# Kernel optimization log

Hardware: AMD Instinct MI355X
Metric: run time of the kernel (lower is better)

Reference implementation:

```python
import jax, jax.numpy as jnp
import numpy as np

B, T = 1, 2048
N_EMBD = 4096
N_HEAD = 32
N_GROUPS = 8
HEAD = 128
Q_PER_KV = N_HEAD // N_GROUPS  # 4
WINDOW = 1024
EPS = 1e-5
ROPE_THETA = 10000.0


def setup_inputs() -> dict:
    key = jax.random.key(0)
    k0, k1, k2 = jax.random.split(key, 3)
    x = jax.random.normal(k0, (B, T, N_EMBD), dtype=jnp.float32)
    # RoPE tables: cos/sin of shape [T, HEAD] (rotary_percentage=1.0)
    inv_freq = 1.0 / (ROPE_THETA ** (jnp.arange(0, HEAD, 2, dtype=jnp.float32) / HEAD))
    ang = jnp.arange(T, dtype=jnp.float32)[:, None] * inv_freq[None, :]  # [T, HEAD//2]
    ang = jnp.concatenate([ang, ang], axis=-1)  # [T, HEAD]
    cos, sin = jnp.cos(ang), jnp.sin(ang)
    qkv_out = (N_HEAD + 2 * N_GROUPS) * HEAD  # 6144
    W_qkv = jax.random.normal(k1, (qkv_out, N_EMBD), dtype=jnp.float32) * 0.02
    W_proj = jax.random.normal(k2, (N_EMBD, N_HEAD * HEAD), dtype=jnp.float32) * 0.02
    norm_q_w = jnp.ones((N_HEAD * HEAD,), dtype=jnp.float32)
    norm_k_w = jnp.ones((N_GROUPS * HEAD,), dtype=jnp.float32)
    return {"x": x, "cos": cos, "sin": sin, "W_qkv": W_qkv,
            "norm_q_w": norm_q_w, "norm_k_w": norm_k_w, "W_proj": W_proj}


def _rmsnorm(x, w):
    # RMSNorm over last dim, matching litgpt RMSNorm (eps inside sqrt)
    var = jnp.mean(x * x, axis=-1, keepdims=True)
    return x * jax.lax.rsqrt(var + EPS) * w


def _apply_rope(x, cos, sin):
    # x: [B, H, T, D]; cos/sin: [T, D] (broadcast over B, H)
    d = x.shape[-1]
    x1, x2 = x[..., : d // 2], x[..., d // 2:]
    rotated = jnp.concatenate([-x2, x1], axis=-1)
    return x * cos + rotated * sin


def reference(x, cos, sin, W_qkv, norm_q_w, norm_k_w, W_proj):
    Bx, Tx, _ = x.shape
    qkv = jnp.einsum('btc,oc->bto', x, W_qkv)  # [B, T, (H+2G)*D]
    q_size = N_HEAD * HEAD
    kv_size = N_GROUPS * HEAD
    q = qkv[..., :q_size]
    k = qkv[..., q_size:q_size + kv_size]
    v = qkv[..., q_size + kv_size:]
    # norm_qk: RMSNorm over the full flattened q / k dims (pre head reshape)
    q = _rmsnorm(q, norm_q_w)
    k = _rmsnorm(k, norm_k_w)
    q = q.reshape(Bx, Tx, N_HEAD, HEAD).transpose(0, 2, 1, 3)     # [B, H, T, D]
    k = k.reshape(Bx, Tx, N_GROUPS, HEAD).transpose(0, 2, 1, 3)   # [B, G, T, D]
    v = v.reshape(Bx, Tx, N_GROUPS, HEAD).transpose(0, 2, 1, 3)   # [B, G, T, D]
    # rope_n_elem == head_size (rotary_percentage = 1.0)
    q = _apply_rope(q, cos, sin)
    k = _apply_rope(k, cos, sin)
    # GQA: expand kv groups to heads (repeat_interleave on head dim)
    k = jnp.repeat(k, Q_PER_KV, axis=1)  # [B, H, T, D]
    v = jnp.repeat(v, Q_PER_KV, axis=1)
    scale = 1.0 / jnp.sqrt(jnp.float32(HEAD))  # attention_scores_scalar is None
    scores = jnp.einsum('bhqd,bhkd->bhqk', q, k) * scale
    # causal + sliding-window mask: allowed iff 0 <= q_idx - kv_idx < WINDOW
    d = jnp.arange(Tx)[:, None] - jnp.arange(Tx)[None, :]
    bias = jnp.where((d >= 0) & (d < WINDOW), 0.0, -jnp.inf).astype(scores.dtype)
    attn = jax.nn.softmax(scores + bias, axis=-1)
    y = jnp.einsum('bhqk,bhkd->bhqd', attn, v)        # [B, H, T, D]
    y = y.transpose(0, 2, 1, 3).reshape(Bx, Tx, N_HEAD * HEAD)
    return jnp.einsum('bth,oh->bto', y, W_proj)       # [B, T, n_embd]
```

## Files before the change

kernel.cpp:

```cpp
#include <hip/hip_runtime.h>
#include <stdint.h>
#include <stddef.h>

#define T_SEQ 2048
#define WINDOW_SZ 1024

typedef __attribute__((ext_vector_type(4))) float f32x4;
typedef __attribute__((ext_vector_type(16))) float f32x16;
typedef __attribute__((ext_vector_type(8))) short s16x8;
typedef __attribute__((ext_vector_type(4))) short s16x4;

__device__ inline unsigned short f2bf(float f) {
  union { float f; unsigned u; } v; v.f = f;
  unsigned u = v.u;
  return (unsigned short)((u + 0x7fffu + ((u >> 16) & 1u)) >> 16);
}
__device__ inline float bf2f(unsigned short u) {
  union { unsigned u; float f; } v; v.u = ((unsigned)u) << 16; return v.f;
}

__device__ inline void gld_lds16(const unsigned short* g, unsigned short* l) {
  __builtin_amdgcn_global_load_lds((const __attribute__((address_space(1))) void*)g,
                                   (__attribute__((address_space(3))) void*)l, 16, 0, 0);
}

__device__ inline void store_out(float* p, float v) { *p = v; }
__device__ inline void store_out(unsigned short* p, float v) { *p = f2bf(v); }

__global__ __launch_bounds__(256) void cvt_all(const float* __restrict__ x,
                                               const float* __restrict__ wqkv,
                                               const float* __restrict__ wproj,
                                               unsigned short* __restrict__ x_bf,
                                               unsigned short* __restrict__ wqkv_bf,
                                               unsigned short* __restrict__ wproj_bf) {
  int i = blockIdx.x * 256 + threadIdx.x;
  const float* s; unsigned short* d; int j;
  if (i < 2097152)       { s = x;     d = x_bf;     j = i; }
  else if (i < 8388608)  { s = wqkv;  d = wqkv_bf;  j = i - 2097152; }
  else                   { s = wproj; d = wproj_bf; j = i - 8388608; }
  float4 v = ((const float4*)s)[j];
  ushort4 o;
  o.x = f2bf(v.x); o.y = f2bf(v.y); o.z = f2bf(v.z); o.w = f2bf(v.w);
  ((ushort4*)d)[j] = o;
}

template <typename OutT>
__global__ __launch_bounds__(256) void gemm_bt(const unsigned short* __restrict__ A,
                                               const unsigned short* __restrict__ Bt,
                                               OutT* __restrict__ C, int M, int N, int K) {
  __shared__ unsigned short As[128 * 64];
  __shared__ unsigned short Bs[128 * 64];
  const int tid  = threadIdx.x;
  const int wave = tid >> 6, lane = tid & 63;
  const int l32 = lane & 31, khalf = lane >> 5;
  const int m0 = blockIdx.y << 7, n0 = blockIdx.x << 7;
  const int wr = (wave >> 1) << 6;
  const int wc = (wave & 1) << 6;
  const int srow = wave * 8 + (lane >> 3);
  const int gchunk0 = lane & 7;

  f32x16 acc[2][2] = {};

  for (int k0 = 0; k0 < K; k0 += 64) {
#pragma unroll
    for (int j = 0; j < 4; j++) {
      int r = j * 32 + srow;
      int gc = gchunk0 ^ (r & 7);
      gld_lds16(A  + (size_t)(m0 + r) * K + k0 + gc * 8, &As[(j * 32 + wave * 8) * 64]);
      gld_lds16(Bt + (size_t)(n0 + r) * K + k0 + gc * 8, &Bs[(j * 32 + wave * 8) * 64]);
    }
    __syncthreads();
#pragma unroll
    for (int s = 0; s < 4; s++) {
      s16x8 af[2], bfr[2];
      int chunk = s * 2 + khalf;
#pragma unroll
      for (int i = 0; i < 2; i++) {
        int ra = wr + i * 32 + l32;
        af[i]  = *(const s16x8*)&As[ra * 64 + ((chunk ^ (ra & 7)) * 8)];
        int rb = wc + i * 32 + l32;
        bfr[i] = *(const s16x8*)&Bs[rb * 64 + ((chunk ^ (rb & 7)) * 8)];
      }
#pragma unroll
      for (int mi = 0; mi < 2; mi++)
#pragma unroll
        for (int ni = 0; ni < 2; ni++)
          acc[mi][ni] = __builtin_amdgcn_mfma_f32_32x32x16_bf16(af[mi], bfr[ni], acc[mi][ni], 0, 0, 0);
    }
    __syncthreads();
  }
#pragma unroll
  for (int mi = 0; mi < 2; mi++)
#pragma unroll
    for (int ni = 0; ni < 2; ni++) {
      int col = n0 + wc + ni * 32 + l32;
      int rbase = m0 + wr + mi * 32 + 4 * khalf;
#pragma unroll
      for (int reg = 0; reg < 16; reg++) {
        int row = rbase + (reg & 3) + 8 * (reg >> 2);
        store_out(&C[(size_t)row * N + col], acc[mi][ni][reg]);
      }
    }
}

__device__ inline void stage_half(const unsigned short* __restrict__ g, int ldk,
                                  int grow0, int k0, unsigned short* lds,
                                  int wave, int lane) {
#pragma unroll
  for (int j = 0; j < 2; j++) {
    int rloc = j * 64 + wave * 8 + (lane >> 3);
    int lc = (lane & 7) ^ (rloc & 7);
    gld_lds16(g + (size_t)(grow0 + rloc) * ldk + k0 + lc * 8,
              lds + (j * 64 + wave * 8) * 64);
  }
}
__device__ inline void stage_64(const unsigned short* __restrict__ g, int ldk,
                                int grow0, int k0, unsigned short* lds,
                                int wave, int lane) {
  int rloc = wave * 8 + (lane >> 3);
  int lc = (lane & 7) ^ (rloc & 7);
  gld_lds16(g + (size_t)(grow0 + rloc) * ldk + k0 + lc * 8,
            lds + (wave * 8) * 64);
}

__global__ __launch_bounds__(512, 2) void gemm256(const unsigned short* __restrict__ A,
                                                  const unsigned short* __restrict__ Bt,
                                                  unsigned short* __restrict__ C,
                                                  int M, int N, int K) {
  __shared__ unsigned short S[73728];
  const int tid = threadIdx.x, wave = tid >> 6, lane = tid & 63;
  const int quad = lane >> 4, l16 = lane & 15;
  const int wm = wave >> 2, wn = wave & 3;
  const int m0 = blockIdx.y << 8, n0 = blockIdx.x * 192;
  const int NT = K >> 6;

  f32x4 acc[8][3] = {};

  unsigned short* const Ab0 = &S[0];
  unsigned short* const Bb0 = &S[49152];

  stage_half(A,  K, m0,       0, Ab0,        wave, lane);
  stage_half(A,  K, m0 + 128, 0, Ab0 + 8192, wave, lane);
  stage_half(Bt, K, n0,       0, Bb0,        wave, lane);
  stage_64  (Bt, K, n0 + 128, 0, Bb0 + 8192, wave, lane);
  if (NT > 1) {
    stage_half(A,  K, m0,       64, Ab0 + 16384,        wave, lane);
    stage_half(A,  K, m0 + 128, 64, Ab0 + 16384 + 8192, wave, lane);
    asm volatile("s_waitcnt vmcnt(4)" ::: "memory");
  } else {
    asm volatile("s_waitcnt vmcnt(0)" ::: "memory");
  }
  __builtin_amdgcn_s_barrier();
  asm volatile("" ::: "memory");

  int ac = 0;
  for (int u = 0; u < NT; ++u) {
    const unsigned short* Sa = Ab0 + ac * 16384;
    const unsigned short* Sb = Bb0 + (u & 1) * 12288;

    if (u + 1 < NT) {
      unsigned short* SbN = Bb0 + ((u + 1) & 1) * 12288;
      stage_half(Bt, K, n0,       (u + 1) << 6, SbN,        wave, lane);
      stage_64  (Bt, K, n0 + 128, (u + 1) << 6, SbN + 8192, wave, lane);
    }
    if (u + 2 < NT) {
      int an2 = ac - 1; if (an2 < 0) an2 = 2;
      unsigned short* SaN = Ab0 + an2 * 16384;
      stage_half(A, K, m0,       (u + 2) << 6, SaN,        wave, lane);
      stage_half(A, K, m0 + 128, (u + 2) << 6, SaN + 8192, wave, lane);
    }

    s16x8 bfr[3][2];
#pragma unroll
    for (int nf = 0; nf < 3; nf++)
#pragma unroll
      for (int ks = 0; ks < 2; ks++) {
        int rb = wn * 48 + nf * 16 + l16;
        bfr[nf][ks] = *(const s16x8*)&Sb[rb * 64 + (((ks * 4 + quad) ^ (rb & 7)) * 8)];
      }
    s16x8 af[8][2];
#pragma unroll
    for (int f = 0; f < 2; f++)
#pragma unroll
      for (int ks = 0; ks < 2; ks++) {
        int ra = wm * 128 + f * 16 + l16;
        af[f][ks] = *(const s16x8*)&Sa[ra * 64 + (((ks * 4 + quad) ^ (ra & 7)) * 8)];
      }
#pragma unroll
    for (int f = 0; f < 8; f++) {
      if (f < 6) {
#pragma unroll
        for (int ks = 0; ks < 2; ks++) {
          int ra = wm * 128 + (f + 2) * 16 + l16;
          af[f + 2][ks] = *(const s16x8*)&Sa[ra * 64 + (((ks * 4 + quad) ^ (ra & 7)) * 8)];
        }
      }
      __builtin_amdgcn_s_setprio(1);
#pragma unroll
      for (int nf = 0; nf < 3; nf++)
#pragma unroll
        for (int ks = 0; ks < 2; ks++)
          acc[f][nf] = __builtin_amdgcn_mfma_f32_16x16x32_bf16(
              af[f][ks], bfr[nf][ks], acc[f][nf], 0, 0, 0);
      __builtin_amdgcn_s_setprio(0);
    }

    if (u + 2 < NT) asm volatile("s_waitcnt vmcnt(4)" ::: "memory");
    else            asm volatile("s_waitcnt vmcnt(0)" ::: "memory");
    asm volatile("" ::: "memory");
    __builtin_amdgcn_s_barrier();
    asm volatile("" ::: "memory");

    ac = (ac == 2) ? 0 : ac + 1;
  }
#pragma unroll
  for (int mf = 0; mf < 8; mf++)
#pragma unroll
    for (int nf = 0; nf < 3; nf++) {
      const int row0 = m0 + wm * 128 + mf * 16 + quad * 4;
      const int col  = n0 + wn * 48 + nf * 16 + l16;
#pragma unroll
      for (int r = 0; r < 4; r++)
        C[(size_t)(row0 + r) * N + col] = f2bf(acc[mf][nf][r]);
    }
}

__global__ __launch_bounds__(256) void normrope(const unsigned short* __restrict__ qkv,
                                                const float* __restrict__ cosb,
                                                const float* __restrict__ sinb,
                                                const float* __restrict__ wq,
                                                const float* __restrict__ wk,
                                                unsigned short* __restrict__ qr,
                                                unsigned short* __restrict__ kr,
                                                unsigned short* __restrict__ vt) {
  const int t = blockIdx.x, tid = threadIdx.x;
  const unsigned short* row = qkv + (size_t)t * 6144;
  float sq = 0.f, sk = 0.f;
  {
    s16x8 a = *(const s16x8*)&row[tid * 16];
    s16x8 b = *(const s16x8*)&row[tid * 16 + 8];
#pragma unroll
    for (int j = 0; j < 8; j++) {
      float fa = bf2f((unsigned short)a[j]), fb = bf2f((unsigned short)b[j]);
      sq += fa * fa + fb * fb;
    }
  }
  {
    s16x4 a = *(const s16x4*)&row[4096 + tid * 4];
#pragma unroll
    for (int j = 0; j < 4; j++) {
      float fa = bf2f((unsigned short)a[j]);
      sk += fa * fa;
    }
  }
#pragma unroll
  for (int off = 32; off; off >>= 1) { sq += __shfl_xor(sq, off); sk += __shfl_xor(sk, off); }
  __shared__ float red[8];
  if ((tid & 63) == 0) { red[tid >> 6] = sq; red[4 + (tid >> 6)] = sk; }
  __syncthreads();
  sq = red[0] + red[1] + red[2] + red[3];
  sk = red[4] + red[5] + red[6] + red[7];
  const float rq = rsqrtf(sq * (1.f / 4096.f) + 1e-5f) * (0.08838834764831845f * 1.4426950408889634f);
  const float rk = rsqrtf(sk * (1.f / 1024.f) + 1e-5f);
  for (int i = tid; i < 4096; i += 256) {
    int h = i >> 7, d = i & 127;
    int pd = (d < 64) ? d + 64 : d - 64;
    float val = bf2f(row[i]) * rq * wq[i];
    float pv  = bf2f(row[(h << 7) + pd]) * rq * wq[(h << 7) + pd];
    float rot = (d < 64) ? -pv : pv;
    float o = val * cosb[t * 128 + d] + rot * sinb[t * 128 + d];
    qr[(size_t)h * T_SEQ * 128 + t * 128 + d] = f2bf(o);
  }
  for (int i = tid; i < 1024; i += 256) {
    int g = i >> 7, d = i & 127;
    int pd = (d < 64) ? d + 64 : d - 64;
    float val = bf2f(row[4096 + i]) * rk * wk[i];
    float pv  = bf2f(row[4096 + (g << 7) + pd]) * rk * wk[(g << 7) + pd];
    float rot = (d < 64) ? -pv : pv;
    float o = val * cosb[t * 128 + d] + rot * sinb[t * 128 + d];
    kr[(size_t)g * T_SEQ * 128 + t * 128 + d] = f2bf(o);
  }
  for (int i = tid; i < 1024; i += 256) {
    int g = i >> 7, d = i & 127;
    vt[(size_t)g * 128 * T_SEQ + (size_t)d * T_SEQ + t] = row[5120 + i];
  }
}

__global__ __launch_bounds__(512, 2) void attn(const unsigned short* __restrict__ Q,
                                               const unsigned short* __restrict__ Kb,
                                               const unsigned short* __restrict__ Vt,
                                               unsigned short* __restrict__ Y) {
  __shared__ unsigned short Kbuf[2][64 * 128];
  __shared__ unsigned short Vbuf[2][128 * 64];
  __shared__ unsigned short Pbuf[8][2][16 * 72];
  const int qb = blockIdx.x, g = blockIdx.y;
  const int tid = threadIdx.x, wave = tid >> 6, lane = tid & 63;
  const int quad = lane >> 4, l16 = lane & 15;
  const int h = g * 4 + (wave >> 1);
  const int qbase = qb * 64;
  const int q0 = qbase + (wave & 1) * 32;
  const unsigned short* Qh = Q + (size_t)h * T_SEQ * 128;
  const unsigned short* Kg = Kb + (size_t)g * T_SEQ * 128;
  const unsigned short* Vg = Vt + (size_t)g * 128 * T_SEQ;

  s16x8 aq[2][4];
#pragma unroll
  for (int qt = 0; qt < 2; qt++)
#pragma unroll
    for (int ks = 0; ks < 4; ks++)
      aq[qt][ks] = *(const s16x8*)&Qh[(size_t)(q0 + qt * 16 + l16) * 128 + ks * 32 + quad * 8];

  f32x4 acc[2][8] = {};
  float lrow[2][4] = {};

  int lo = qbase - (WINDOW_SZ - 1);
  if (lo < 0) lo = 0;
  lo &= ~63;

#define STAGE_CHUNK(buf, kkv)                                                        \
  {                                                                                  \
    int kk_ = (kkv);                                                                 \
    _Pragma("unroll")                                                                \
    for (int j = 0; j < 2; j++) {                                                    \
      int rloc = wave * 8 + j * 4 + (lane >> 4);                                     \
      int oct = (lane & 15) ^ (rloc & 15);                                           \
      gld_lds16(Kg + (size_t)(kk_ + rloc) * 128 + oct * 8,                           \
                &Kbuf[buf][(wave * 8 + j * 4) * 128]);                               \
    }                                                                                \
    _Pragma("unroll")                                                                \
    for (int j = 0; j < 2; j++) {                                                    \
      int dloc = wave * 16 + j * 8 + (lane >> 3);                                    \
      int oct = (lane & 7) ^ (dloc & 7);                                             \
      gld_lds16(Vg + (size_t)dloc * T_SEQ + kk_ + oct * 8,                           \
                &Vbuf[buf][(wave * 16 + j * 8) * 64]);                               \
    }                                                                                \
  }

  STAGE_CHUNK(0, lo);
  int ib = 0;
  for (int kk = lo; kk < qbase + 64; kk += 64, ib ^= 1) {
    __syncthreads();
    if (kk + 64 < qbase + 64) STAGE_CHUNK(ib ^ 1, kk + 64);
    if (kk > q0 + 31 || kk + 63 < q0 - (WINDOW_SZ - 1)) continue;
    const unsigned short* kb = Kbuf[ib];
    const unsigned short* vb = Vbuf[ib];
    f32x4 sc[2][4] = {};
    __builtin_amdgcn_s_setprio(1);
#pragma unroll
    for (int ks = 0; ks < 4; ks++) {
#pragma unroll
      for (int ci = 0; ci < 4; ci++) {
        s16x8 bk = *(const s16x8*)&kb[(ci * 16 + l16) * 128 + (((ks * 4 + quad) ^ l16) * 8)];
        sc[0][ci] = __builtin_amdgcn_mfma_f32_16x16x32_bf16(aq[0][ks], bk, sc[0][ci], 0, 0, 0);
        sc[1][ci] = __builtin_amdgcn_mfma_f32_16x16x32_bf16(aq[1][ks], bk, sc[1][ci], 0, 0, 0);
      }
    }
    __builtin_amdgcn_s_setprio(0);
#pragma unroll
    for (int qt = 0; qt < 2; qt++)
#pragma unroll
      for (int ci = 0; ci < 4; ci++) {
        int col = kk + ci * 16 + l16;
#pragma unroll
        for (int r = 0; r < 4; r++) {
          int irow = q0 + qt * 16 + quad * 4 + r;
          unsigned dd = (unsigned)(irow - col);
          float e = (dd < (unsigned)WINDOW_SZ) ? exp2f(sc[qt][ci][r]) : 0.f;
          lrow[qt][r] += e;
          Pbuf[wave][qt][(quad * 4 + r) * 72 + ci * 16 + l16] = f2bf(e);
        }
      }
    __builtin_amdgcn_s_setprio(1);
#pragma unroll
    for (int c = 0; c < 2; c++) {
      s16x8 pa0 = *(const s16x8*)&Pbuf[wave][0][l16 * 72 + c * 32 + quad * 8];
      s16x8 pa1 = *(const s16x8*)&Pbuf[wave][1][l16 * 72 + c * 32 + quad * 8];
#pragma unroll
      for (int n = 0; n < 8; n++) {
        s16x8 bv = *(const s16x8*)&vb[(n * 16 + l16) * 64 + (((c * 4 + quad) ^ (l16 & 7)) * 8)];
        acc[0][n] = __builtin_amdgcn_mfma_f32_16x16x32_bf16(pa0, bv, acc[0][n], 0, 0, 0);
        acc[1][n] = __builtin_amdgcn_mfma_f32_16x16x32_bf16(pa1, bv, acc[1][n], 0, 0, 0);
      }
    }
    __builtin_amdgcn_s_setprio(0);
  }
#undef STAGE_CHUNK
#pragma unroll
  for (int qt = 0; qt < 2; qt++)
#pragma unroll
    for (int r = 0; r < 4; r++) {
#pragma unroll
      for (int off = 8; off; off >>= 1) lrow[qt][r] += __shfl_xor(lrow[qt][r], off);
      lrow[qt][r] = 1.f / lrow[qt][r];
    }
#pragma unroll
  for (int qt = 0; qt < 2; qt++)
#pragma unroll
    for (int n = 0; n < 8; n++)
#pragma unroll
      for (int r = 0; r < 4; r++) {
        int irow = q0 + qt * 16 + quad * 4 + r;
        Y[(size_t)irow * 4096 + h * 128 + n * 16 + l16] = f2bf(acc[qt][n][r] * lrow[qt][r]);
      }
}

extern "C" void kernel_launch(void* const* d_in, const int* in_sizes, int n_in,
                              void* d_out, int out_size, void* d_ws, size_t ws_size,
                              hipStream_t stream) {
  (void)in_sizes; (void)n_in; (void)out_size; (void)ws_size;
  const float* x     = (const float*)d_in[0];
  const float* cosb  = (const float*)d_in[1];
  const float* sinb  = (const float*)d_in[2];
  const float* Wqkv  = (const float*)d_in[3];
  const float* wq    = (const float*)d_in[4];
  const float* wk    = (const float*)d_in[5];
  const float* Wproj = (const float*)d_in[6];
  float* out = (float*)d_out;

  char* ws = (char*)d_ws;
  unsigned short* x_bf     = (unsigned short*)(ws);
  unsigned short* wqkv_bf  = (unsigned short*)(ws + 16777216);
  unsigned short* wproj_bf = (unsigned short*)(ws + 67108864);
  unsigned short* qkv      = (unsigned short*)(ws + 100663296);
  unsigned short* qr       = (unsigned short*)(ws + 150994944);
  unsigned short* kr       = (unsigned short*)(ws + 167772160);
  unsigned short* vt       = (unsigned short*)(ws + 171966464);
  unsigned short* y        = (unsigned short*)(ws + 176160768);

  cvt_all<<<49152, 256, 0, stream>>>(x, Wqkv, Wproj, x_bf, wqkv_bf, wproj_bf);
  gemm256<<<dim3(32, 8), 512, 0, stream>>>(x_bf, wqkv_bf, qkv, 2048, 6144, 4096);
  normrope<<<2048, 256, 0, stream>>>(qkv, cosb, sinb, wq, wk, qr, kr, vt);
  attn<<<dim3(32, 8), 512, 0, stream>>>(qr, kr, vt, y);
  gemm_bt<float><<<dim3(32, 16), 256, 0, stream>>>(y, wproj_bf, out, 2048, 4096, 4096);
}
```

Before: 477.1 us.

## Replace output projection GEMM with pipelined 128x256-tile MFMA kernel

The simple 128x128 single-buffered output-projection GEMM is replaced by a 512-thread kernel with 128x256 tiles. B is triple-buffered and A double-buffered through async global-to-LDS loads, with explicit vmcnt waits and raw barriers so loads for later k-steps overlap the MFMAs of the current one. It uses 16x16x32 MFMAs with setprio around the compute and launches 256 blocks instead of 512. The goal is to hide memory latency and raise MFMA utilisation, at the cost of 128KB of LDS per block, which may limit occupancy.

```diff
diff --git a/kernel.cpp b/kernel.cpp
--- a/kernel.cpp
+++ b/kernel.cpp
@@ -23,9 +23,6 @@
   __builtin_amdgcn_global_load_lds((const __attribute__((address_space(1))) void*)g,
                                    (__attribute__((address_space(3))) void*)l, 16, 0, 0);
 }
-
-__device__ inline void store_out(float* p, float v) { *p = v; }
-__device__ inline void store_out(unsigned short* p, float v) { *p = f2bf(v); }
 
 __global__ __launch_bounds__(256) void cvt_all(const float* __restrict__ x,
                                                const float* __restrict__ wqkv,
@@ -44,65 +41,6 @@
   ((ushort4*)d)[j] = o;
 }
 
-template <typename OutT>
-__global__ __launch_bounds__(256) void gemm_bt(const unsigned short* __restrict__ A,
-                                               const unsigned short* __restrict__ Bt,
-                                               OutT* __restrict__ C, int M, int N, int K) {
-  __shared__ unsigned short As[128 * 64];
-  __shared__ unsigned short Bs[128 * 64];
-  const int tid  = threadIdx.x;
-  const int wave = tid >> 6, lane = tid & 63;
-  const int l32 = lane & 31, khalf = lane >> 5;
-  const int m0 = blockIdx.y << 7, n0 = blockIdx.x << 7;
-  const int wr = (wave >> 1) << 6;
-  const int wc = (wave & 1) << 6;
-  const int srow = wave * 8 + (lane >> 3);
-  const int gchunk0 = lane & 7;
-
-  f32x16 acc[2][2] = {};
-
-  for (int k0 = 0; k0 < K; k0 += 64) {
-#pragma unroll
-    for (int j = 0; j < 4; j++) {
-      int r = j * 32 + srow;
-      int gc = gchunk0 ^ (r & 7);
-      gld_lds16(A  + (size_t)(m0 + r) * K + k0 + gc * 8, &As[(j * 32 + wave * 8) * 64]);
-      gld_lds16(Bt + (size_t)(n0 + r) * K + k0 + gc * 8, &Bs[(j * 32 + wave * 8) * 64]);
-    }
-    __syncthreads();
-#pragma unroll
-    for (int s = 0; s < 4; s++) {
-      s16x8 af[2], bfr[2];
-      int chunk = s * 2 + khalf;
-#pragma unroll
-      for (int i = 0; i < 2; i++) {
-        int ra = wr + i * 32 + l32;
-        af[i]  = *(const s16x8*)&As[ra * 64 + ((chunk ^ (ra & 7)) * 8)];
-        int rb = wc + i * 32 + l32;
-        bfr[i] = *(const s16x8*)&Bs[rb * 64 + ((chunk ^ (rb & 7)) * 8)];
-      }
-#pragma unroll
-      for (int mi = 0; mi < 2; mi++)
-#pragma unroll
-        for (int ni = 0; ni < 2; ni++)
-          acc[mi][ni] = __builtin_amdgcn_mfma_f32_32x32x16_bf16(af[mi], bfr[ni], acc[mi][ni], 0, 0, 0);
-    }
-    __syncthreads();
-  }
-#pragma unroll
-  for (int mi = 0; mi < 2; mi++)
-#pragma unroll
-    for (int ni = 0; ni < 2; ni++) {
-      int col = n0 + wc + ni * 32 + l32;
-      int rbase = m0 + wr + mi * 32 + 4 * khalf;
-#pragma unroll
-      for (int reg = 0; reg < 16; reg++) {
-        int row = rbase + (reg & 3) + 8 * (reg >> 2);
-        store_out(&C[(size_t)row * N + col], acc[mi][ni][reg]);
-      }
-    }
-}
-
 __device__ inline void stage_half(const unsigned short* __restrict__ g, int ldk,
                                   int grow0, int k0, unsigned short* lds,
                                   int wave, int lane) {
@@ -222,6 +160,102 @@
 #pragma unroll
       for (int r = 0; r < 4; r++)
         C[(size_t)(row0 + r) * N + col] = f2bf(acc[mf][nf][r]);
+    }
+}
+
+__global__ __launch_bounds__(512, 2) void gemm256p(const unsigned short* __restrict__ A,
+                                                   const unsigned short* __restrict__ Bt,
+                                                   float* __restrict__ C,
+                                                   int M, int N, int K) {
+  __shared__ unsigned short S[65536];
+  const int tid = threadIdx.x, wave = tid >> 6, lane = tid & 63;
+  const int quad = lane >> 4, l16 = lane & 15;
+  const int wm = wave >> 2, wn = wave & 3;
+  const int m0 = blockIdx.y << 7, n0 = blockIdx.x << 8;
+  const int NT = K >> 6;
+
+  f32x4 acc[4][4] = {};
+
+  unsigned short* const Bb0 = &S[0];
+  unsigned short* const Ab0 = &S[49152];
+
+  stage_half(A,  K, m0,       0, Ab0,        wave, lane);
+  stage_half(Bt, K, n0,       0, Bb0,        wave, lane);
+  stage_half(Bt, K, n0 + 128, 0, Bb0 + 8192, wave, lane);
+  if (NT > 1) {
+    stage_half(Bt, K, n0,       64, Bb0 + 16384,        wave, lane);
+    stage_half(Bt, K, n0 + 128, 64, Bb0 + 16384 + 8192, wave, lane);
+    asm volatile("s_waitcnt vmcnt(4)" ::: "memory");
+  } else {
+    asm volatile("s_waitcnt vmcnt(0)" ::: "memory");
+  }
+  __builtin_amdgcn_s_barrier();
+  asm volatile("" ::: "memory");
+
+  int bc = 0;
+  for (int u = 0; u < NT; ++u) {
+    const unsigned short* Sb = Bb0 + bc * 16384;
+    const unsigned short* Sa = Ab0 + (u & 1) * 8192;
+
+    if (u + 1 < NT)
+      stage_half(A, K, m0, (u + 1) << 6, Ab0 + ((u + 1) & 1) * 8192, wave, lane);
+    if (u + 2 < NT) {
+      int bn2 = bc - 1; if (bn2 < 0) bn2 = 2;
+      unsigned short* SbN = Bb0 + bn2 * 16384;
+      stage_half(Bt, K, n0,       (u + 2) << 6, SbN,        wave, lane);
+      stage_half(Bt, K, n0 + 128, (u + 2) << 6, SbN + 8192, wave, lane);
+    }
+
+    s16x8 bfr[4][2];
+#pragma unroll
+    for (int nf = 0; nf < 4; nf++)
+#pragma unroll
+      for (int ks = 0; ks < 2; ks++) {
+        int rb = wn * 64 + nf * 16 + l16;
+        bfr[nf][ks] = *(const s16x8*)&Sb[rb * 64 + (((ks * 4 + quad) ^ (rb & 7)) * 8)];
+      }
+    s16x8 af[4][2];
+#pragma unroll
+    for (int ks = 0; ks < 2; ks++) {
+      int ra = wm * 64 + l16;
+      af[0][ks] = *(const s16x8*)&Sa[ra * 64 + (((ks * 4 + quad) ^ (ra & 7)) * 8)];
+    }
+#pragma unroll
+    for (int mf = 0; mf < 4; mf++) {
+      if (mf < 3) {
+#pragma unroll
+        for (int ks = 0; ks < 2; ks++) {
+          int ra = wm * 64 + (mf + 1) * 16 + l16;
+          af[mf + 1][ks] = *(const s16x8*)&Sa[ra * 64 + (((ks * 4 + quad) ^ (ra & 7)) * 8)];
+        }
+      }
+      __builtin_amdgcn_s_setprio(1);
+#pragma unroll
+      for (int nf = 0; nf < 4; nf++)
+#pragma unroll
+        for (int ks = 0; ks < 2; ks++)
+          acc[mf][nf] = __builtin_amdgcn_mfma_f32_16x16x32_bf16(
+              af[mf][ks], bfr[nf][ks], acc[mf][nf], 0, 0, 0);
+      __builtin_amdgcn_s_setprio(0);
+    }
+
+    if (u + 2 < NT) asm volatile("s_waitcnt vmcnt(4)" ::: "memory");
+    else            asm volatile("s_waitcnt vmcnt(0)" ::: "memory");
+    asm volatile("" ::: "memory");
+    __builtin_amdgcn_s_barrier();
+    asm volatile("" ::: "memory");
+
+    bc = (bc == 2) ? 0 : bc + 1;
+  }
+#pragma unroll
+  for (int mf = 0; mf < 4; mf++)
+#pragma unroll
+    for (int nf = 0; nf < 4; nf++) {
+      const int row0 = m0 + wm * 64 + mf * 16 + quad * 4;
+      const int col  = n0 + wn * 64 + nf * 16 + l16;
+#pragma unroll
+      for (int r = 0; r < 4; r++)
+        C[(size_t)(row0 + r) * N + col] = acc[mf][nf][r];
     }
 }
 
@@ -431,5 +465,5 @@
   gemm256<<<dim3(32, 8), 512, 0, stream>>>(x_bf, wqkv_bf, qkv, 2048, 6144, 4096);
   normrope<<<2048, 256, 0, stream>>>(qkv, cosb, sinb, wq, wk, qr, kr, vt);
   attn<<<dim3(32, 8), 512, 0, stream>>>(qr, kr, vt, y);
-  gemm_bt<float><<<dim3(32, 16), 256, 0, stream>>>(y, wproj_bf, out, 2048, 4096, 4096);
-}
+  gemm256p<<<dim3(16, 16), 512, 0, stream>>>(y, wproj_bf, out, 2048, 4096, 4096);
+}
```

After: 463.1 us. 2.9% less time.
